# Kernel optimization log

Hardware: AMD Instinct MI355X
Metric: run time of the kernel (lower is better)

The kernel has to match this reference:

```python
import jax, jax.numpy as jnp
import numpy as np

B = 4096          # number of graphs
NPG = 148         # nodes per graph (fixed by ReadOut(num_nodes=148))
N = B * NPG       # total nodes = 606208
EPG = 592         # edges per graph (~avg degree 4: RNA backbone + base pairs)
E = B * EPG       # total edges = 2424832


def setup_inputs() -> dict:
    key = jax.random.key(0)
    ks = jax.random.split(key, 10)
    x = jax.random.normal(ks[0], (N, 4), jnp.float32)
    # edges confined within each graph via per-graph node offsets
    src = jax.random.randint(ks[1], (E,), 0, NPG, dtype=jnp.int32)
    dst = jax.random.randint(ks[2], (E,), 0, NPG, dtype=jnp.int32)
    offs = jnp.repeat(jnp.arange(B, dtype=jnp.int32) * NPG, EPG)
    edge_index = jnp.stack([src + offs, dst + offs], axis=0)
    batch = jnp.repeat(jnp.arange(B, dtype=jnp.int32), NPG)
    # GCNConv weights (glorot-ish) and biases: 4->16->32->64
    def glorot(k, fi, fo):
        return jax.random.normal(k, (fi, fo), jnp.float32) * np.sqrt(2.0 / (fi + fo)).astype(np.float32)
    W1 = glorot(ks[3], 4, 16); b1 = jnp.zeros((16,), jnp.float32)
    W2 = glorot(ks[4], 16, 32); b2 = jnp.zeros((32,), jnp.float32)
    W3 = glorot(ks[5], 32, 64); b3 = jnp.zeros((64,), jnp.float32)
    return {"x": x, "edge_index": edge_index, "batch": batch,
            "W1": W1, "b1": b1, "W2": W2, "b2": b2, "W3": W3, "b3": b3}


def gcn_conv(x, src, dst, W, b, n):
    """PyG GCNConv: x' = D^{-1/2}(A+I)D^{-1/2} (x W) + b."""
    h = x @ W                                   # [n, out]
    loop = jnp.arange(n, dtype=src.dtype)       # self loops
    s = jnp.concatenate([src, loop])
    d = jnp.concatenate([dst, loop])
    deg = jax.ops.segment_sum(jnp.ones_like(s, h.dtype), d, num_segments=n)
    dis = jnp.where(deg > 0, jax.lax.rsqrt(jnp.maximum(deg, 1e-12)), 0.0)
    norm = dis[s] * dis[d]                      # [n_edges_with_loops]
    msg = h[s] * norm[:, None]                  # gather + normalize
    return jax.ops.segment_sum(msg, d, num_segments=n) + b


def reference(x, edge_index, batch, W1, b1, W2, b2, W3, b3):
    src, dst = edge_index[0], edge_index[1]
    n = x.shape[0]
    # Dropout(p=0.1) is identity at inference time
    h = jax.nn.relu(gcn_conv(x, src, dst, W1, b1, n))
    h = jax.nn.relu(gcn_conv(h, src, dst, W2, b2, n))
    h = jax.nn.relu(gcn_conv(h, src, dst, W3, b3, n))
    # to_dense_batch with max_num_nodes=148: every graph has exactly 148 nodes
    # and `batch` is sorted block-constant, so dense batching == reshape.
    dense = h.reshape(B, NPG, h.shape[-1])      # [B, 148, 64]
    return dense.reshape(B, -1)                 # Flatten -> [B, 9472]
```

## Files before the change

### kernel.cpp

```cpp
#include <hip/hip_runtime.h>

#define NPG 148
#define EPG 592
#define NTHR 256
#define SA   40
#define MT   10

typedef _Float16 h8 __attribute__((ext_vector_type(8)));
typedef _Float16 h4 __attribute__((ext_vector_type(4)));
typedef float    f4 __attribute__((ext_vector_type(4)));

__device__ __forceinline__ float f16bits_to_f32(unsigned short u) {
    return (float)__builtin_bit_cast(_Float16, u);
}


template<int Fi, int Fo, int KC, int NTN, int MAXJ, int WROW, int BOFF, bool LAST>
__device__ __forceinline__ void layer(int t,
    _Float16* __restrict__ A16, const _Float16* __restrict__ Wt,
    const _Float16* __restrict__ s_bh, const unsigned int* __restrict__ s_csr,
    const unsigned short* __restrict__ s_row, const unsigned short* __restrict__ s_dis,
    float* __restrict__ gout)
{
    float a[KC][8];
    if (t < NPG) {
        const float dd = f16bits_to_f32(s_dis[t]);
        const char* selfb = reinterpret_cast<const char*>(A16) + t * (SA * 2);
        #pragma unroll
        for (int kc = 0; kc < KC; ++kc) {
            const h8 hv = *reinterpret_cast<const h8*>(selfb + kc * 16);
            #pragma unroll
            for (int u = 0; u < 8; ++u) a[kc][u] = dd * (float)hv[u];
        }
        int e  = s_row[t];
        const int e1 = s_row[t + 1];
        unsigned int pk = (e < e1) ? s_csr[e] : 0u;
        while (e < e1) {
            const unsigned int pknext = (e + 1 < e1) ? s_csr[e + 1] : 0u;
            const char* mb = reinterpret_cast<const char*>(A16) + (pk & 0xffffu);
            const float ds = f16bits_to_f32((unsigned short)(pk >> 16));
            #pragma unroll
            for (int kc = 0; kc < KC; ++kc) {
                const h8 m = *reinterpret_cast<const h8*>(mb + kc * 16);
                #pragma unroll
                for (int u = 0; u < 8; ++u) a[kc][u] = fmaf((float)m[u], ds, a[kc][u]);
            }
            pk = pknext;
            ++e;
        }
        #pragma unroll
        for (int kc = 0; kc < KC; ++kc)
            #pragma unroll
            for (int u = 0; u < 8; ++u) a[kc][u] *= dd;
    }
    __syncthreads();
    if (t < NPG) {
        char* selfb = reinterpret_cast<char*>(A16) + t * (SA * 2);
        #pragma unroll
        for (int kc = 0; kc < KC; ++kc) {
            h8 pv;
            #pragma unroll
            for (int u = 0; u < 8; ++u) pv[u] = (_Float16)a[kc][u];
            *reinterpret_cast<h8*>(selfb + kc * 16) = pv;
        }
    }
    __syncthreads();

    const int w   = t >> 6;
    const int l16 = t & 15;
    const int q   = (t >> 4) & 3;
    h8 af[MAXJ], bf[MAXJ];
    #pragma unroll
    for (int j = 0; j < MAXJ; ++j) {
        const int idx = w + 4 * j;
        if (idx < MT * NTN) {
            const int mt = idx / NTN, nt = idx % NTN;
            af[j] = *reinterpret_cast<const h8*>(&A16[(mt * 16 + l16) * SA + q * 8]);
            bf[j] = *reinterpret_cast<const h8*>(&Wt[(WROW + nt * 16 + l16) * SA + q * 8]);
        }
    }
    __syncthreads();
    #pragma unroll
    for (int j = 0; j < MAXJ; ++j) {
        const int idx = w + 4 * j;
        if (idx < MT * NTN) {
            const int mt = idx / NTN, nt = idx % NTN;
            f4 acc = {0.f, 0.f, 0.f, 0.f};
            acc = __builtin_amdgcn_mfma_f32_16x16x32_f16(af[j], bf[j], acc, 0, 0, 0);
            const int col  = nt * 16 + l16;
            const float bias = (float)s_bh[BOFF + col];
            #pragma unroll
            for (int rr = 0; rr < 4; ++rr) {
                const float v = fmaxf(acc[rr] + bias, 0.f);
                const int row = mt * 16 + q * 4 + rr;
                if (LAST) {
                    if (row < NPG) gout[row * 64 + col] = v;
                } else {
                    A16[row * SA + col] = (_Float16)v;
                }
            }
        }
    }
    if (!LAST) __syncthreads();
}

__global__ __launch_bounds__(256, 6)
void gcn_fused(const float* __restrict__ x,
               const int* __restrict__ esrc, const int* __restrict__ edst,
               const float* __restrict__ W1, const float* __restrict__ b1,
               const float* __restrict__ W2, const float* __restrict__ b2,
               const float* __restrict__ W3, const float* __restrict__ b3,
               float* __restrict__ out)
{
    __shared__ __align__(16) _Float16 A16[160 * SA];
    __shared__ __align__(16) _Float16 Wt[112 * SA];
    __shared__ _Float16 s_bh[112];
    __shared__ unsigned int s_csr[EPG];
    __shared__ unsigned short s_row[152];
    __shared__ unsigned short s_dis[NPG];
    __shared__ int s_cnt[NPG], s_cnt2[NPG];

    int* s_edge = reinterpret_cast<int*>(Wt);

    const int t  = threadIdx.x;
    const int g  = blockIdx.x;
    const int be = g * EPG;
    const int bn = g * NPG;

    if (t < NPG) { s_cnt[t] = 0; s_cnt2[t] = 0; }
    for (int e = t; e < EPG; e += NTHR) {
        const int s = esrc[be + e] - bn;
        const int d = edst[be + e] - bn;
        s_edge[e] = s | (d << 8);
    }
    __syncthreads();

    for (int e = t; e < EPG; e += NTHR)
        atomicAdd(&s_cnt[((unsigned)s_edge[e]) >> 8], 1);
    __syncthreads();

    if (t < NPG) {
        const float disf = rsqrtf((float)(s_cnt[t] + 1));
        s_dis[t] = __builtin_bit_cast(unsigned short, (_Float16)disf);
    }
    if (t < 64) {
        const int lane = t;
        int v0 = s_cnt[lane];
        int v1 = s_cnt[64 + lane];
        int v2 = (128 + lane < NPG) ? s_cnt[128 + lane] : 0;
        #pragma unroll
        for (int off = 1; off < 64; off <<= 1) {
            const int u0 = __shfl_up(v0, off);
            const int u1 = __shfl_up(v1, off);
            const int u2 = __shfl_up(v2, off);
            if (lane >= off) { v0 += u0; v1 += u1; v2 += u2; }
        }
        const int t0 = __shfl(v0, 63);
        const int t1 = __shfl(v1, 63);
        v1 += t0;
        v2 += t0 + t1;
        if (lane == 0) s_row[0] = 0;
        s_row[1 + lane]  = (unsigned short)v0;
        s_row[65 + lane] = (unsigned short)v1;
        if (128 + lane < NPG) s_row[129 + lane] = (unsigned short)v2;
    }
    __syncthreads();

    for (int e = t; e < EPG; e += NTHR) {
        const int pk = s_edge[e];
        const int s  = pk & 0xFF;
        const int d  = (unsigned)pk >> 8;
        const int pos = (int)s_row[d] + atomicAdd(&s_cnt2[d], 1);
        s_csr[pos] = (unsigned int)(s * (SA * 2)) | ((unsigned int)s_dis[s] << 16);
    }
    __syncthreads();

    for (int i = t; i < 160 * SA / 8; i += NTHR) reinterpret_cast<f4*>(A16)[i] = f4{0.f, 0.f, 0.f, 0.f};
    for (int i = t; i < 112 * SA / 8; i += NTHR) reinterpret_cast<f4*>(Wt)[i]  = f4{0.f, 0.f, 0.f, 0.f};
    __syncthreads();
    for (int i = t; i < 64;   i += NTHR) Wt[(i & 15) * SA + (i >> 4)]        = (_Float16)W1[i];
    for (int i = t; i < 512;  i += NTHR) Wt[(16 + (i & 31)) * SA + (i >> 5)] = (_Float16)W2[i];
    for (int i = t; i < 2048; i += NTHR) Wt[(48 + (i & 63)) * SA + (i >> 6)] = (_Float16)W3[i];
    if (t < 16)       s_bh[t] = (_Float16)b1[t];
    else if (t < 48)  s_bh[t] = (_Float16)b2[t - 16];
    else if (t < 112) s_bh[t] = (_Float16)b3[t - 48];
    if (t < NPG) {
        const float4 xv = reinterpret_cast<const float4*>(x)[bn + t];
        h4 p; p[0] = (_Float16)xv.x; p[1] = (_Float16)xv.y; p[2] = (_Float16)xv.z; p[3] = (_Float16)xv.w;
        *reinterpret_cast<h4*>(&A16[t * SA]) = p;
    }
    __syncthreads();

    float* gout = out + (size_t)bn * 64;
    layer< 4, 16,  1,  1,   3,    0,   0, false>(t, A16, Wt, s_bh, s_csr, s_row, s_dis, gout);
    layer<16, 32,  2,  2,   5,   16,  16, false>(t, A16, Wt, s_bh, s_csr, s_row, s_dis, gout);
    layer<32, 64,  4,  4,  10,   48,  48, true >(t, A16, Wt, s_bh, s_csr, s_row, s_dis, gout);
}

extern "C" void kernel_launch(void* const* d_in, const int* in_sizes, int n_in,
                              void* d_out, int out_size, void* d_ws, size_t ws_size,
                              hipStream_t stream)
{
    const float* x  = (const float*)d_in[0];
    const int*   ei = (const int*)d_in[1];
    const float* W1 = (const float*)d_in[3];
    const float* b1 = (const float*)d_in[4];
    const float* W2 = (const float*)d_in[5];
    const float* b2 = (const float*)d_in[6];
    const float* W3 = (const float*)d_in[7];
    const float* b3 = (const float*)d_in[8];
    float* out = (float*)d_out;

    const int N = in_sizes[0] / 4;
    const int B = N / NPG;
    const int E = in_sizes[1] / 2;

    gcn_fused<<<B, NTHR, 0, stream>>>(x, ei, ei + E, W1, b1, W2, b2, W3, b3, out);
}
```

Before: 64.96 us.

## Aggregate neighbors directly into MFMA fragments and overlap weight staging with CSR build

Each thread now gathers and normalizes one node's 8-feature chunk straight into the MFMA A-fragment registers. This removes the intermediate write-back of aggregated features to shared memory and two barriers per layer. Weight loading is restructured so each B fragment is loaded once per column tile and reused across the M tiles, and the activation row stride shrinks from 40 to 36 halves. Zeroing and loading W1/W2, biases and x are moved ahead of the CSR build, and W3 loading happens without a separate barrier. The risks are relying on the layer-1 barriers to order the W3 writes, possible bank conflicts at the new stride, and uneven gather work across lanes.

```diff
diff --git a/kernel.cpp b/kernel.cpp
--- a/kernel.cpp
+++ b/kernel.cpp
@@ -3,100 +3,84 @@
 #define NPG 148
 #define EPG 592
 #define NTHR 256
-#define SA   40
+#define SA   36
+#define SW   40
 #define MT   10
 
 typedef _Float16 h8 __attribute__((ext_vector_type(8)));
 typedef _Float16 h4 __attribute__((ext_vector_type(4)));
 typedef float    f4 __attribute__((ext_vector_type(4)));
 
-__device__ __forceinline__ float f16bits_to_f32(unsigned short u) {
+__device__ __forceinline__ float f16b(unsigned short u) {
     return (float)__builtin_bit_cast(_Float16, u);
 }
 
 
-template<int Fi, int Fo, int KC, int NTN, int MAXJ, int WROW, int BOFF, bool LAST>
+template<int Fi, int Fo, int NTN, int WROW, int BOFF, bool LAST>
 __device__ __forceinline__ void layer(int t,
     _Float16* __restrict__ A16, const _Float16* __restrict__ Wt,
     const _Float16* __restrict__ s_bh, const unsigned int* __restrict__ s_csr,
     const unsigned short* __restrict__ s_row, const unsigned short* __restrict__ s_dis,
     float* __restrict__ gout)
 {
-    float a[KC][8];
-    if (t < NPG) {
-        const float dd = f16bits_to_f32(s_dis[t]);
-        const char* selfb = reinterpret_cast<const char*>(A16) + t * (SA * 2);
-        #pragma unroll
-        for (int kc = 0; kc < KC; ++kc) {
-            const h8 hv = *reinterpret_cast<const h8*>(selfb + kc * 16);
-            #pragma unroll
-            for (int u = 0; u < 8; ++u) a[kc][u] = dd * (float)hv[u];
-        }
-        int e  = s_row[t];
-        const int e1 = s_row[t + 1];
-        unsigned int pk = (e < e1) ? s_csr[e] : 0u;
-        while (e < e1) {
-            const unsigned int pknext = (e + 1 < e1) ? s_csr[e + 1] : 0u;
-            const char* mb = reinterpret_cast<const char*>(A16) + (pk & 0xffffu);
-            const float ds = f16bits_to_f32((unsigned short)(pk >> 16));
-            #pragma unroll
-            for (int kc = 0; kc < KC; ++kc) {
-                const h8 m = *reinterpret_cast<const h8*>(mb + kc * 16);
-                #pragma unroll
-                for (int u = 0; u < 8; ++u) a[kc][u] = fmaf((float)m[u], ds, a[kc][u]);
-            }
-            pk = pknext;
-            ++e;
-        }
-        #pragma unroll
-        for (int kc = 0; kc < KC; ++kc)
-            #pragma unroll
-            for (int u = 0; u < 8; ++u) a[kc][u] *= dd;
-    }
-    __syncthreads();
-    if (t < NPG) {
-        char* selfb = reinterpret_cast<char*>(A16) + t * (SA * 2);
-        #pragma unroll
-        for (int kc = 0; kc < KC; ++kc) {
-            h8 pv;
-            #pragma unroll
-            for (int u = 0; u < 8; ++u) pv[u] = (_Float16)a[kc][u];
-            *reinterpret_cast<h8*>(selfb + kc * 16) = pv;
-        }
-    }
-    __syncthreads();
-
     const int w   = t >> 6;
     const int l16 = t & 15;
     const int q   = (t >> 4) & 3;
-    h8 af[MAXJ], bf[MAXJ];
+    constexpr int KQA = (Fi + 7) / 8;
+
+    h8 af[3];
+    const char* baseq = reinterpret_cast<const char*>(A16) + q * 16;
     #pragma unroll
-    for (int j = 0; j < MAXJ; ++j) {
-        const int idx = w + 4 * j;
-        if (idx < MT * NTN) {
-            const int mt = idx / NTN, nt = idx % NTN;
-            af[j] = *reinterpret_cast<const h8*>(&A16[(mt * 16 + l16) * SA + q * 8]);
-            bf[j] = *reinterpret_cast<const h8*>(&Wt[(WROW + nt * 16 + l16) * SA + q * 8]);
+    for (int j = 0; j < 3; ++j) {
+        h8 z = {(_Float16)0, (_Float16)0, (_Float16)0, (_Float16)0,
+                (_Float16)0, (_Float16)0, (_Float16)0, (_Float16)0};
+        af[j] = z;
+        const int mt   = w + 4 * j;
+        const int node = mt * 16 + l16;
+        if (mt < MT && q < KQA && node < NPG) {
+            const float dd = f16b(s_dis[node]);
+            const h8 hv = *reinterpret_cast<const h8*>(baseq + node * (SA * 2));
+            float a[8];
+            #pragma unroll
+            for (int u = 0; u < 8; ++u) a[u] = dd * (float)hv[u];
+            int e = s_row[node];
+            const int e1 = s_row[node + 1];
+            unsigned int pk = (e < e1) ? s_csr[e] : 0u;
+            while (e < e1) {
+                const unsigned int pn = (e + 1 < e1) ? s_csr[e + 1] : 0u;
+                const h8 m = *reinterpret_cast<const h8*>(baseq + (pk & 0xffffu));
+                const float ds = f16b((unsigned short)(pk >> 16));
+                #pragma unroll
+                for (int u = 0; u < 8; ++u) a[u] = fmaf((float)m[u], ds, a[u]);
+                pk = pn;
+                ++e;
+            }
+            #pragma unroll
+            for (int u = 0; u < 8; ++u) af[j][u] = (_Float16)(a[u] * dd);
         }
     }
     __syncthreads();
+
     #pragma unroll
-    for (int j = 0; j < MAXJ; ++j) {
-        const int idx = w + 4 * j;
-        if (idx < MT * NTN) {
-            const int mt = idx / NTN, nt = idx % NTN;
-            f4 acc = {0.f, 0.f, 0.f, 0.f};
-            acc = __builtin_amdgcn_mfma_f32_16x16x32_f16(af[j], bf[j], acc, 0, 0, 0);
-            const int col  = nt * 16 + l16;
-            const float bias = (float)s_bh[BOFF + col];
-            #pragma unroll
-            for (int rr = 0; rr < 4; ++rr) {
-                const float v = fmaxf(acc[rr] + bias, 0.f);
-                const int row = mt * 16 + q * 4 + rr;
-                if (LAST) {
-                    if (row < NPG) gout[row * 64 + col] = v;
-                } else {
-                    A16[row * SA + col] = (_Float16)v;
+    for (int nt = 0; nt < NTN; ++nt) {
+        const h8 bf = *reinterpret_cast<const h8*>(&Wt[(WROW + nt * 16 + l16) * SW + q * 8]);
+        const int col = nt * 16 + l16;
+        const float bias = (float)s_bh[BOFF + col];
+        #pragma unroll
+        for (int j = 0; j < 3; ++j) {
+            const int mt = w + 4 * j;
+            if (mt < MT) {
+                f4 acc = {0.f, 0.f, 0.f, 0.f};
+                acc = __builtin_amdgcn_mfma_f32_16x16x32_f16(af[j], bf, acc, 0, 0, 0);
+                #pragma unroll
+                for (int rr = 0; rr < 4; ++rr) {
+                    const float v = fmaxf(acc[rr] + bias, 0.f);
+                    const int row = mt * 16 + q * 4 + rr;
+                    if (LAST) {
+                        if (row < NPG) gout[row * 64 + col] = v;
+                    } else {
+                        A16[row * SA + col] = (_Float16)v;
+                    }
                 }
             }
         }
@@ -113,20 +97,35 @@
                float* __restrict__ out)
 {
     __shared__ __align__(16) _Float16 A16[160 * SA];
-    __shared__ __align__(16) _Float16 Wt[112 * SA];
+    __shared__ __align__(16) _Float16 Wt[112 * SW];
     __shared__ _Float16 s_bh[112];
     __shared__ unsigned int s_csr[EPG];
     __shared__ unsigned short s_row[152];
-    __shared__ unsigned short s_dis[NPG];
+    __shared__ unsigned short s_dis[148];
     __shared__ int s_cnt[NPG], s_cnt2[NPG];
 
-    int* s_edge = reinterpret_cast<int*>(Wt);
+    int* s_edge = reinterpret_cast<int*>(Wt + 48 * SW);
 
     const int t  = threadIdx.x;
     const int g  = blockIdx.x;
     const int be = g * EPG;
     const int bn = g * NPG;
 
+    for (int i = t; i < 160 * SA / 8; i += NTHR)
+        reinterpret_cast<f4*>(A16)[i] = f4{0.f, 0.f, 0.f, 0.f};
+    for (int i = t; i < 224; i += NTHR) {
+        const int r = i / 14, c = 2 + i % 14;
+        reinterpret_cast<unsigned int*>(Wt)[r * (SW / 2) + c] = 0u;
+    }
+    for (int i = t; i < 256; i += NTHR) {
+        const int r = 16 + i / 8, c = 8 + i % 8;
+        reinterpret_cast<unsigned int*>(Wt)[r * (SW / 2) + c] = 0u;
+    }
+    for (int i = t; i < 64;  i += NTHR) Wt[(i & 15) * SW + (i >> 4)]        = (_Float16)W1[i];
+    for (int i = t; i < 512; i += NTHR) Wt[(16 + (i & 31)) * SW + (i >> 5)] = (_Float16)W2[i];
+    if (t < 16)       s_bh[t] = (_Float16)b1[t];
+    else if (t < 48)  s_bh[t] = (_Float16)b2[t - 16];
+    else if (t < 112) s_bh[t] = (_Float16)b3[t - 48];
     if (t < NPG) { s_cnt[t] = 0; s_cnt2[t] = 0; }
     for (int e = t; e < EPG; e += NTHR) {
         const int s = esrc[be + e] - bn;
@@ -142,6 +141,9 @@
     if (t < NPG) {
         const float disf = rsqrtf((float)(s_cnt[t] + 1));
         s_dis[t] = __builtin_bit_cast(unsigned short, (_Float16)disf);
+        const float4 xv = reinterpret_cast<const float4*>(x)[bn + t];
+        h4 p; p[0] = (_Float16)xv.x; p[1] = (_Float16)xv.y; p[2] = (_Float16)xv.z; p[3] = (_Float16)xv.w;
+        *reinterpret_cast<h4*>(&A16[t * SA]) = p;
     }
     if (t < 64) {
         const int lane = t;
@@ -175,26 +177,13 @@
     }
     __syncthreads();
 
-    for (int i = t; i < 160 * SA / 8; i += NTHR) reinterpret_cast<f4*>(A16)[i] = f4{0.f, 0.f, 0.f, 0.f};
-    for (int i = t; i < 112 * SA / 8; i += NTHR) reinterpret_cast<f4*>(Wt)[i]  = f4{0.f, 0.f, 0.f, 0.f};
-    __syncthreads();
-    for (int i = t; i < 64;   i += NTHR) Wt[(i & 15) * SA + (i >> 4)]        = (_Float16)W1[i];
-    for (int i = t; i < 512;  i += NTHR) Wt[(16 + (i & 31)) * SA + (i >> 5)] = (_Float16)W2[i];
-    for (int i = t; i < 2048; i += NTHR) Wt[(48 + (i & 63)) * SA + (i >> 6)] = (_Float16)W3[i];
-    if (t < 16)       s_bh[t] = (_Float16)b1[t];
-    else if (t < 48)  s_bh[t] = (_Float16)b2[t - 16];
-    else if (t < 112) s_bh[t] = (_Float16)b3[t - 48];
-    if (t < NPG) {
-        const float4 xv = reinterpret_cast<const float4*>(x)[bn + t];
-        h4 p; p[0] = (_Float16)xv.x; p[1] = (_Float16)xv.y; p[2] = (_Float16)xv.z; p[3] = (_Float16)xv.w;
-        *reinterpret_cast<h4*>(&A16[t * SA]) = p;
-    }
-    __syncthreads();
+    for (int i = t; i < 2048; i += NTHR)
+        Wt[(48 + (i & 63)) * SW + (i >> 6)] = (_Float16)W3[i];
 
     float* gout = out + (size_t)bn * 64;
-    layer< 4, 16,  1,  1,   3,    0,   0, false>(t, A16, Wt, s_bh, s_csr, s_row, s_dis, gout);
-    layer<16, 32,  2,  2,   5,   16,  16, false>(t, A16, Wt, s_bh, s_csr, s_row, s_dis, gout);
-    layer<32, 64,  4,  4,  10,   48,  48, true >(t, A16, Wt, s_bh, s_csr, s_row, s_dis, gout);
+    layer< 4, 16,  1,    0,   0, false>(t, A16, Wt, s_bh, s_csr, s_row, s_dis, gout);
+    layer<16, 32,  2,   16,  16, false>(t, A16, Wt, s_bh, s_csr, s_row, s_dis, gout);
+    layer<32, 64,  4,   48,  48, true >(t, A16, Wt, s_bh, s_csr, s_row, s_dis, gout);
 }
 
 extern "C" void kernel_launch(void* const* d_in, const int* in_sizes, int n_in,
```

Result: slower. 83.03 us (+27.8%).

## Degree-sort aggregation threads, use packed fp16 math, and merge setup phases

Applied to the files above, without the earlier changes.

Aggregation now runs in packed fp16 vector arithmetic instead of per-element fp32 FMAs. Nodes are reassigned to threads in degree-sorted order through a counting sort (s_meta), which aims to cut wavefront divergence in the edge loop. The setup phases are reorganised: edges are kept in registers, weight and x loading overlaps with degree counting, and several barriers are dropped. The A16 row stride shrinks to 36 halves, which changes the LDS bank pattern. fp16 accumulation loses precision compared with the previous fp32 accumulation.

```diff
diff --git a/kernel.cpp b/kernel.cpp
--- a/kernel.cpp
+++ b/kernel.cpp
@@ -3,66 +3,59 @@
 #define NPG 148
 #define EPG 592
 #define NTHR 256
-#define SA   40
+#define SA   36
+#define SW   40
 #define MT   10
 
 typedef _Float16 h8 __attribute__((ext_vector_type(8)));
 typedef _Float16 h4 __attribute__((ext_vector_type(4)));
 typedef float    f4 __attribute__((ext_vector_type(4)));
-
-__device__ __forceinline__ float f16bits_to_f32(unsigned short u) {
-    return (float)__builtin_bit_cast(_Float16, u);
+typedef unsigned int u32;
+
+__device__ __forceinline__ h8 bcast_pk(u32 p) {
+    uint4 q = {p, p, p, p};
+    return __builtin_bit_cast(h8, q);
 }
 
 
 template<int Fi, int Fo, int KC, int NTN, int MAXJ, int WROW, int BOFF, bool LAST>
 __device__ __forceinline__ void layer(int t,
     _Float16* __restrict__ A16, const _Float16* __restrict__ Wt,
-    const _Float16* __restrict__ s_bh, const unsigned int* __restrict__ s_csr,
-    const unsigned short* __restrict__ s_row, const unsigned short* __restrict__ s_dis,
-    float* __restrict__ gout)
+    const _Float16* __restrict__ s_bh, const u32* __restrict__ s_csr,
+    const uint2* __restrict__ s_meta, float* __restrict__ gout)
 {
-    float a[KC][8];
-    if (t < NPG) {
-        const float dd = f16bits_to_f32(s_dis[t]);
-        const char* selfb = reinterpret_cast<const char*>(A16) + t * (SA * 2);
-        #pragma unroll
-        for (int kc = 0; kc < KC; ++kc) {
-            const h8 hv = *reinterpret_cast<const h8*>(selfb + kc * 16);
+    h8 a[KC];
+    int off_self = 0;
+    if (t < NPG) {
+        const uint2 me = s_meta[t];
+        off_self = (int)(me.x & 0xffffu);
+        const h8 ddv = bcast_pk((me.x & 0xffff0000u) | (me.x >> 16));
+        const char* base = reinterpret_cast<const char*>(A16) + off_self;
+        #pragma unroll
+        for (int kc = 0; kc < KC; ++kc)
+            a[kc] = *reinterpret_cast<const h8*>(base + kc * 16) * ddv;
+        int e = (int)(me.y & 0xffffu);
+        const int e1 = (int)(me.y >> 16);
+        u32 pk = (e < e1) ? s_csr[e] : 0u;
+        while (e < e1) {
+            const u32 pn = (e + 1 < e1) ? s_csr[e + 1] : 0u;
+            const char* mb = reinterpret_cast<const char*>(A16) + (pk & 0xffffu);
+            const h8 dsv = bcast_pk((pk & 0xffff0000u) | (pk >> 16));
             #pragma unroll
-            for (int u = 0; u < 8; ++u) a[kc][u] = dd * (float)hv[u];
-        }
-        int e  = s_row[t];
-        const int e1 = s_row[t + 1];
-        unsigned int pk = (e < e1) ? s_csr[e] : 0u;
-        while (e < e1) {
-            const unsigned int pknext = (e + 1 < e1) ? s_csr[e + 1] : 0u;
-            const char* mb = reinterpret_cast<const char*>(A16) + (pk & 0xffffu);
-            const float ds = f16bits_to_f32((unsigned short)(pk >> 16));
-            #pragma unroll
-            for (int kc = 0; kc < KC; ++kc) {
-                const h8 m = *reinterpret_cast<const h8*>(mb + kc * 16);
-                #pragma unroll
-                for (int u = 0; u < 8; ++u) a[kc][u] = fmaf((float)m[u], ds, a[kc][u]);
-            }
-            pk = pknext;
+            for (int kc = 0; kc < KC; ++kc)
+                a[kc] += *reinterpret_cast<const h8*>(mb + kc * 16) * dsv;
+            pk = pn;
             ++e;
         }
         #pragma unroll
+        for (int kc = 0; kc < KC; ++kc) a[kc] *= ddv;
+    }
+    __syncthreads();
+    if (t < NPG) {
+        char* base = reinterpret_cast<char*>(A16) + off_self;
+        #pragma unroll
         for (int kc = 0; kc < KC; ++kc)
-            #pragma unroll
-            for (int u = 0; u < 8; ++u) a[kc][u] *= dd;
-    }
-    __syncthreads();
-    if (t < NPG) {
-        char* selfb = reinterpret_cast<char*>(A16) + t * (SA * 2);
-        #pragma unroll
-        for (int kc = 0; kc < KC; ++kc) {
-            h8 pv;
-            #pragma unroll
-            for (int u = 0; u < 8; ++u) pv[u] = (_Float16)a[kc][u];
-            *reinterpret_cast<h8*>(selfb + kc * 16) = pv;
-        }
+            *reinterpret_cast<h8*>(base + kc * 16) = a[kc];
     }
     __syncthreads();
 
@@ -76,7 +69,7 @@
         if (idx < MT * NTN) {
             const int mt = idx / NTN, nt = idx % NTN;
             af[j] = *reinterpret_cast<const h8*>(&A16[(mt * 16 + l16) * SA + q * 8]);
-            bf[j] = *reinterpret_cast<const h8*>(&Wt[(WROW + nt * 16 + l16) * SA + q * 8]);
+            bf[j] = *reinterpret_cast<const h8*>(&Wt[(WROW + nt * 16 + l16) * SW + q * 8]);
         }
     }
     __syncthreads();
@@ -113,36 +106,60 @@
                float* __restrict__ out)
 {
     __shared__ __align__(16) _Float16 A16[160 * SA];
-    __shared__ __align__(16) _Float16 Wt[112 * SA];
+    __shared__ __align__(16) _Float16 Wt[112 * SW];
     __shared__ _Float16 s_bh[112];
-    __shared__ unsigned int s_csr[EPG];
+    __shared__ u32 s_csr[EPG];
     __shared__ unsigned short s_row[152];
     __shared__ unsigned short s_dis[NPG];
+    __shared__ uint2 s_meta[NPG];
     __shared__ int s_cnt[NPG], s_cnt2[NPG];
-
-    int* s_edge = reinterpret_cast<int*>(Wt);
+    __shared__ int s_hist[64], s_boff[64], s_bcnt[64];
 
     const int t  = threadIdx.x;
     const int g  = blockIdx.x;
     const int be = g * EPG;
     const int bn = g * NPG;
 
+    for (int i = t; i < 160 * SA / 8; i += NTHR)
+        reinterpret_cast<f4*>(A16)[i] = f4{0.f, 0.f, 0.f, 0.f};
+    for (int i = t; i < 112 * SW / 8; i += NTHR)
+        reinterpret_cast<f4*>(Wt)[i] = f4{0.f, 0.f, 0.f, 0.f};
     if (t < NPG) { s_cnt[t] = 0; s_cnt2[t] = 0; }
-    for (int e = t; e < EPG; e += NTHR) {
-        const int s = esrc[be + e] - bn;
-        const int d = edst[be + e] - bn;
-        s_edge[e] = s | (d << 8);
-    }
-    __syncthreads();
-
-    for (int e = t; e < EPG; e += NTHR)
-        atomicAdd(&s_cnt[((unsigned)s_edge[e]) >> 8], 1);
-    __syncthreads();
-
-    if (t < NPG) {
-        const float disf = rsqrtf((float)(s_cnt[t] + 1));
-        s_dis[t] = __builtin_bit_cast(unsigned short, (_Float16)disf);
-    }
+    if (t < 64)  { s_hist[t] = 0; s_bcnt[t] = 0; }
+    __syncthreads();
+
+    u32 epk[3];
+    #pragma unroll
+    for (int k = 0; k < 3; ++k) {
+        const int e = t + k * NTHR;
+        epk[k] = 0xffffffffu;
+        if (e < EPG) {
+            const int s = esrc[be + e] - bn;
+            const int d = edst[be + e] - bn;
+            epk[k] = (u32)(s | (d << 8));
+            atomicAdd(&s_cnt[d], 1);
+        }
+    }
+    for (int i = t; i < 64;   i += NTHR) Wt[(i & 15) * SW + (i >> 4)]        = (_Float16)W1[i];
+    for (int i = t; i < 512;  i += NTHR) Wt[(16 + (i & 31)) * SW + (i >> 5)] = (_Float16)W2[i];
+    for (int i = t; i < 2048; i += NTHR) Wt[(48 + (i & 63)) * SW + (i >> 6)] = (_Float16)W3[i];
+    if (t < 16)       s_bh[t] = (_Float16)b1[t];
+    else if (t < 48)  s_bh[t] = (_Float16)b2[t - 16];
+    else if (t < 112) s_bh[t] = (_Float16)b3[t - 48];
+    if (t < NPG) {
+        const float4 xv = reinterpret_cast<const float4*>(x)[bn + t];
+        h4 p; p[0] = (_Float16)xv.x; p[1] = (_Float16)xv.y; p[2] = (_Float16)xv.z; p[3] = (_Float16)xv.w;
+        *reinterpret_cast<h4*>(&A16[t * SA]) = p;
+    }
+    __syncthreads();
+
+    if (t < NPG) {
+        const int deg = s_cnt[t];
+        s_dis[t] = __builtin_bit_cast(unsigned short, (_Float16)rsqrtf((float)(deg + 1)));
+        atomicAdd(&s_hist[min(deg, 63)], 1);
+    }
+    __syncthreads();
+
     if (t < 64) {
         const int lane = t;
         int v0 = s_cnt[lane];
@@ -163,38 +180,41 @@
         s_row[1 + lane]  = (unsigned short)v0;
         s_row[65 + lane] = (unsigned short)v1;
         if (128 + lane < NPG) s_row[129 + lane] = (unsigned short)v2;
-    }
-    __syncthreads();
-
-    for (int e = t; e < EPG; e += NTHR) {
-        const int pk = s_edge[e];
-        const int s  = pk & 0xFF;
-        const int d  = (unsigned)pk >> 8;
-        const int pos = (int)s_row[d] + atomicAdd(&s_cnt2[d], 1);
-        s_csr[pos] = (unsigned int)(s * (SA * 2)) | ((unsigned int)s_dis[s] << 16);
-    }
-    __syncthreads();
-
-    for (int i = t; i < 160 * SA / 8; i += NTHR) reinterpret_cast<f4*>(A16)[i] = f4{0.f, 0.f, 0.f, 0.f};
-    for (int i = t; i < 112 * SA / 8; i += NTHR) reinterpret_cast<f4*>(Wt)[i]  = f4{0.f, 0.f, 0.f, 0.f};
-    __syncthreads();
-    for (int i = t; i < 64;   i += NTHR) Wt[(i & 15) * SA + (i >> 4)]        = (_Float16)W1[i];
-    for (int i = t; i < 512;  i += NTHR) Wt[(16 + (i & 31)) * SA + (i >> 5)] = (_Float16)W2[i];
-    for (int i = t; i < 2048; i += NTHR) Wt[(48 + (i & 63)) * SA + (i >> 6)] = (_Float16)W3[i];
-    if (t < 16)       s_bh[t] = (_Float16)b1[t];
-    else if (t < 48)  s_bh[t] = (_Float16)b2[t - 16];
-    else if (t < 112) s_bh[t] = (_Float16)b3[t - 48];
-    if (t < NPG) {
-        const float4 xv = reinterpret_cast<const float4*>(x)[bn + t];
-        h4 p; p[0] = (_Float16)xv.x; p[1] = (_Float16)xv.y; p[2] = (_Float16)xv.z; p[3] = (_Float16)xv.w;
-        *reinterpret_cast<h4*>(&A16[t * SA]) = p;
+    } else if (t < 128) {
+        const int lane = t - 64;
+        const int orig = s_hist[lane];
+        int v = orig;
+        #pragma unroll
+        for (int off = 1; off < 64; off <<= 1) {
+            const int u = __shfl_up(v, off);
+            if (lane >= off) v += u;
+        }
+        s_boff[lane] = v - orig;
+    }
+    __syncthreads();
+
+    #pragma unroll
+    for (int k = 0; k < 3; ++k) {
+        if (epk[k] != 0xffffffffu) {
+            const int s = epk[k] & 0xff;
+            const int d = (epk[k] >> 8) & 0xff;
+            const int pos = (int)s_row[d] + atomicAdd(&s_cnt2[d], 1);
+            s_csr[pos] = (u32)(s * (SA * 2)) | ((u32)s_dis[s] << 16);
+        }
+    }
+    if (t < NPG) {
+        const int deg = s_cnt[t];
+        const int b   = min(deg, 63);
+        const int p   = s_boff[b] + atomicAdd(&s_bcnt[b], 1);
+        s_meta[p] = make_uint2((u32)(t * (SA * 2)) | ((u32)s_dis[t] << 16),
+                               (u32)s_row[t] | ((u32)s_row[t + 1] << 16));
     }
     __syncthreads();
 
     float* gout = out + (size_t)bn * 64;
-    layer< 4, 16,  1,  1,   3,    0,   0, false>(t, A16, Wt, s_bh, s_csr, s_row, s_dis, gout);
-    layer<16, 32,  2,  2,   5,   16,  16, false>(t, A16, Wt, s_bh, s_csr, s_row, s_dis, gout);
-    layer<32, 64,  4,  4,  10,   48,  48, true >(t, A16, Wt, s_bh, s_csr, s_row, s_dis, gout);
+    layer< 4, 16,  1,  1,   3,    0,   0, false>(t, A16, Wt, s_bh, s_csr, s_meta, gout);
+    layer<16, 32,  2,  2,   5,   16,  16, false>(t, A16, Wt, s_bh, s_csr, s_meta, gout);
+    layer<32, 64,  4,  4,  10,   48,  48, true >(t, A16, Wt, s_bh, s_csr, s_meta, gout);
 }
 
 extern "C" void kernel_launch(void* const* d_in, const int* in_sizes, int n_in,
```

New measurement: 108.9 us. 1.68x slower.

## Process two graphs per block and merge setup phases to cut barriers

Applied to the files above, without the earlier changes.

Each 512-thread block now handles two graphs, one per 256-thread half, so the weight transpose and bias loads are shared across two graphs. Edge packing and degree counting are fused into one pass that keeps the packed edges in registers, and the separate zeroing and weight-load phases are merged, which removes several block-wide barriers. The activation row stride drops to 36 halves, presumably to change the LDS bank pattern and cut footprint. The risks are that 16-byte vector LDS accesses on 72-byte rows are no longer 16-byte aligned, that barriers now stall both graphs together, and that the larger LDS footprint per block could lower occupancy.

```diff
diff --git a/kernel.cpp b/kernel.cpp
--- a/kernel.cpp
+++ b/kernel.cpp
@@ -2,50 +2,53 @@
 
 #define NPG 148
 #define EPG 592
-#define NTHR 256
-#define SA   40
+#define NTHR 512
+#define GPB  2
+#define SA   36
+#define SW   40
 #define MT   10
 
 typedef _Float16 h8 __attribute__((ext_vector_type(8)));
 typedef _Float16 h4 __attribute__((ext_vector_type(4)));
 typedef float    f4 __attribute__((ext_vector_type(4)));
-
-__device__ __forceinline__ float f16bits_to_f32(unsigned short u) {
+typedef unsigned int u32;
+
+__device__ __forceinline__ float f16b(unsigned short u) {
     return (float)__builtin_bit_cast(_Float16, u);
 }
 
 
 template<int Fi, int Fo, int KC, int NTN, int MAXJ, int WROW, int BOFF, bool LAST>
-__device__ __forceinline__ void layer(int t,
+__device__ __forceinline__ void layer(int tl,
     _Float16* __restrict__ A16, const _Float16* __restrict__ Wt,
-    const _Float16* __restrict__ s_bh, const unsigned int* __restrict__ s_csr,
+    const _Float16* __restrict__ s_bh, const u32* __restrict__ s_csr,
     const unsigned short* __restrict__ s_row, const unsigned short* __restrict__ s_dis,
     float* __restrict__ gout)
 {
     float a[KC][8];
-    if (t < NPG) {
-        const float dd = f16bits_to_f32(s_dis[t]);
-        const char* selfb = reinterpret_cast<const char*>(A16) + t * (SA * 2);
+    if (tl < NPG) {
+        const float dd = f16b(s_dis[tl]);
+        const char* selfb = reinterpret_cast<const char*>(A16) + tl * (SA * 2);
         #pragma unroll
         for (int kc = 0; kc < KC; ++kc) {
             const h8 hv = *reinterpret_cast<const h8*>(selfb + kc * 16);
             #pragma unroll
             for (int u = 0; u < 8; ++u) a[kc][u] = dd * (float)hv[u];
         }
-        int e  = s_row[t];
-        const int e1 = s_row[t + 1];
-        unsigned int pk = (e < e1) ? s_csr[e] : 0u;
+        int e  = s_row[tl];
+        const int e1 = s_row[tl + 1];
+        u32 pk = (e < e1) ? s_csr[e] : 0u;
         while (e < e1) {
-            const unsigned int pknext = (e + 1 < e1) ? s_csr[e + 1] : 0u;
+            const u32 pn = (e + 1 < e1) ? s_csr[e + 1] : 0u;
             const char* mb = reinterpret_cast<const char*>(A16) + (pk & 0xffffu);
-            const float ds = f16bits_to_f32((unsigned short)(pk >> 16));
+            const float ds = f16b((unsigned short)(pk >> 16));
             #pragma unroll
             for (int kc = 0; kc < KC; ++kc) {
                 const h8 m = *reinterpret_cast<const h8*>(mb + kc * 16);
                 #pragma unroll
                 for (int u = 0; u < 8; ++u) a[kc][u] = fmaf((float)m[u], ds, a[kc][u]);
             }
-            pk = pknext;
+            pk = pn;
             ++e;
         }
         #pragma unroll
@@ -54,8 +57,8 @@
             for (int u = 0; u < 8; ++u) a[kc][u] *= dd;
     }
     __syncthreads();
-    if (t < NPG) {
-        char* selfb = reinterpret_cast<char*>(A16) + t * (SA * 2);
+    if (tl < NPG) {
+        char* selfb = reinterpret_cast<char*>(A16) + tl * (SA * 2);
         #pragma unroll
         for (int kc = 0; kc < KC; ++kc) {
             h8 pv;
@@ -66,9 +69,9 @@
     }
     __syncthreads();
 
-    const int w   = t >> 6;
-    const int l16 = t & 15;
-    const int q   = (t >> 4) & 3;
+    const int w   = tl >> 6;
+    const int l16 = tl & 15;
+    const int q   = (tl >> 4) & 3;
     h8 af[MAXJ], bf[MAXJ];
     #pragma unroll
     for (int j = 0; j < MAXJ; ++j) {
@@ -76,7 +79,7 @@
         if (idx < MT * NTN) {
             const int mt = idx / NTN, nt = idx % NTN;
             af[j] = *reinterpret_cast<const h8*>(&A16[(mt * 16 + l16) * SA + q * 8]);
-            bf[j] = *reinterpret_cast<const h8*>(&Wt[(WROW + nt * 16 + l16) * SA + q * 8]);
+            bf[j] = *reinterpret_cast<const h8*>(&Wt[(WROW + nt * 16 + l16) * SW + q * 8]);
         }
     }
     __syncthreads();
@@ -104,7 +107,7 @@
     if (!LAST) __syncthreads();
 }
 
-__global__ __launch_bounds__(256, 6)
+__global__ __launch_bounds__(NTHR, 8)
 void gcn_fused(const float* __restrict__ x,
                const int* __restrict__ esrc, const int* __restrict__ edst,
                const float* __restrict__ W1, const float* __restrict__ b1,
@@ -112,42 +115,61 @@
                const float* __restrict__ W3, const float* __restrict__ b3,
                float* __restrict__ out)
 {
-    __shared__ __align__(16) _Float16 A16[160 * SA];
-    __shared__ __align__(16) _Float16 Wt[112 * SA];
+    __shared__ __align__(16) _Float16 A16[GPB][160 * SA];
+    __shared__ __align__(16) _Float16 Wt[112 * SW];
     __shared__ _Float16 s_bh[112];
-    __shared__ unsigned int s_csr[EPG];
-    __shared__ unsigned short s_row[152];
-    __shared__ unsigned short s_dis[NPG];
-    __shared__ int s_cnt[NPG], s_cnt2[NPG];
-
-    int* s_edge = reinterpret_cast<int*>(Wt);
+    __shared__ u32 s_csr[GPB][EPG];
+    __shared__ unsigned short s_row[GPB][152];
+    __shared__ unsigned short s_dis[GPB][NPG];
+    __shared__ int s_cnt[GPB][NPG], s_cnt2[GPB][NPG];
 
     const int t  = threadIdx.x;
-    const int g  = blockIdx.x;
+    const int gl = t >> 8;
+    const int tl = t & 255;
+    const int g  = blockIdx.x * GPB + gl;
     const int be = g * EPG;
     const int bn = g * NPG;
 
-    if (t < NPG) { s_cnt[t] = 0; s_cnt2[t] = 0; }
-    for (int e = t; e < EPG; e += NTHR) {
-        const int s = esrc[be + e] - bn;
-        const int d = edst[be + e] - bn;
-        s_edge[e] = s | (d << 8);
-    }
-    __syncthreads();
-
-    for (int e = t; e < EPG; e += NTHR)
-        atomicAdd(&s_cnt[((unsigned)s_edge[e]) >> 8], 1);
-    __syncthreads();
-
-    if (t < NPG) {
-        const float disf = rsqrtf((float)(s_cnt[t] + 1));
-        s_dis[t] = __builtin_bit_cast(unsigned short, (_Float16)disf);
-    }
-    if (t < 64) {
-        const int lane = t;
-        int v0 = s_cnt[lane];
-        int v1 = s_cnt[64 + lane];
-        int v2 = (128 + lane < NPG) ? s_cnt[128 + lane] : 0;
+    for (int i = t; i < GPB * 160 * SA / 8; i += NTHR)
+        reinterpret_cast<f4*>(&A16[0][0])[i] = f4{0.f, 0.f, 0.f, 0.f};
+    for (int i = t; i < 112 * SW / 8; i += NTHR)
+        reinterpret_cast<f4*>(Wt)[i] = f4{0.f, 0.f, 0.f, 0.f};
+    if (tl < NPG) { s_cnt[gl][tl] = 0; s_cnt2[gl][tl] = 0; }
+    __syncthreads();
+
+    u32 epk[3];
+    #pragma unroll
+    for (int k = 0; k < 3; ++k) {
+        const int e = tl + k * 256;
+        epk[k] = 0xffffffffu;
+        if (e < EPG) {
+            const int s = esrc[be + e] - bn;
+            const int d = edst[be + e] - bn;
+            epk[k] = (u32)(s | (d << 8));
+            atomicAdd(&s_cnt[gl][d], 1);
+        }
+    }
+    for (int i = t; i < 64;   i += NTHR) Wt[(i & 15) * SW + (i >> 4)]        = (_Float16)W1[i];
+    for (int i = t; i < 512;  i += NTHR) Wt[(16 + (i & 31)) * SW + (i >> 5)] = (_Float16)W2[i];
+    for (int i = t; i < 2048; i += NTHR) Wt[(48 + (i & 63)) * SW + (i >> 6)] = (_Float16)W3[i];
+    if (t < 16)       s_bh[t] = (_Float16)b1[t];
+    else if (t < 48)  s_bh[t] = (_Float16)b2[t - 16];
+    else if (t < 112) s_bh[t] = (_Float16)b3[t - 48];
+    if (tl < NPG) {
+        const float4 xv = reinterpret_cast<const float4*>(x)[bn + tl];
+        h4 p; p[0] = (_Float16)xv.x; p[1] = (_Float16)xv.y; p[2] = (_Float16)xv.z; p[3] = (_Float16)xv.w;
+        *reinterpret_cast<h4*>(&A16[gl][tl * SA]) = p;
+    }
+    __syncthreads();
+
+    if (tl < NPG)
+        s_dis[gl][tl] = __builtin_bit_cast(unsigned short,
+                                           (_Float16)rsqrtf((float)(s_cnt[gl][tl] + 1)));
+    if (tl < 64) {
+        const int lane = tl;
+        int v0 = s_cnt[gl][lane];
+        int v1 = s_cnt[gl][64 + lane];
+        int v2 = (128 + lane < NPG) ? s_cnt[gl][128 + lane] : 0;
         #pragma unroll
         for (int off = 1; off < 64; off <<= 1) {
             const int u0 = __shfl_up(v0, off);
@@ -159,42 +181,28 @@
         const int t1 = __shfl(v1, 63);
         v1 += t0;
         v2 += t0 + t1;
-        if (lane == 0) s_row[0] = 0;
-        s_row[1 + lane]  = (unsigned short)v0;
-        s_row[65 + lane] = (unsigned short)v1;
-        if (128 + lane < NPG) s_row[129 + lane] = (unsigned short)v2;
-    }
-    __syncthreads();
-
-    for (int e = t; e < EPG; e += NTHR) {
-        const int pk = s_edge[e];
-        const int s  = pk & 0xFF;
-        const int d  = (unsigned)pk >> 8;
-        const int pos = (int)s_row[d] + atomicAdd(&s_cnt2[d], 1);
-        s_csr[pos] = (unsigned int)(s * (SA * 2)) | ((unsigned int)s_dis[s] << 16);
-    }
-    __syncthreads();
-
-    for (int i = t; i < 160 * SA / 8; i += NTHR) reinterpret_cast<f4*>(A16)[i] = f4{0.f, 0.f, 0.f, 0.f};
-    for (int i = t; i < 112 * SA / 8; i += NTHR) reinterpret_cast<f4*>(Wt)[i]  = f4{0.f, 0.f, 0.f, 0.f};
-    __syncthreads();
-    for (int i = t; i < 64;   i += NTHR) Wt[(i & 15) * SA + (i >> 4)]        = (_Float16)W1[i];
-    for (int i = t; i < 512;  i += NTHR) Wt[(16 + (i & 31)) * SA + (i >> 5)] = (_Float16)W2[i];
-    for (int i = t; i < 2048; i += NTHR) Wt[(48 + (i & 63)) * SA + (i >> 6)] = (_Float16)W3[i];
-    if (t < 16)       s_bh[t] = (_Float16)b1[t];
-    else if (t < 48)  s_bh[t] = (_Float16)b2[t - 16];
-    else if (t < 112) s_bh[t] = (_Float16)b3[t - 48];
-    if (t < NPG) {
-        const float4 xv = reinterpret_cast<const float4*>(x)[bn + t];
-        h4 p; p[0] = (_Float16)xv.x; p[1] = (_Float16)xv.y; p[2] = (_Float16)xv.z; p[3] = (_Float16)xv.w;
-        *reinterpret_cast<h4*>(&A16[t * SA]) = p;
+        if (lane == 0) s_row[gl][0] = 0;
+        s_row[gl][1 + lane]  = (unsigned short)v0;
+        s_row[gl][65 + lane] = (unsigned short)v1;
+        if (128 + lane < NPG) s_row[gl][129 + lane] = (unsigned short)v2;
+    }
+    __syncthreads();
+
+    #pragma unroll
+    for (int k = 0; k < 3; ++k) {
+        if (epk[k] != 0xffffffffu) {
+            const int s = epk[k] & 0xff;
+            const int d = (epk[k] >> 8) & 0xff;
+            const int pos = (int)s_row[gl][d] + atomicAdd(&s_cnt2[gl][d], 1);
+            s_csr[gl][pos] = (u32)(s * (SA * 2)) | ((u32)s_dis[gl][s] << 16);
+        }
     }
     __syncthreads();
 
     float* gout = out + (size_t)bn * 64;
-    layer< 4, 16,  1,  1,   3,    0,   0, false>(t, A16, Wt, s_bh, s_csr, s_row, s_dis, gout);
-    layer<16, 32,  2,  2,   5,   16,  16, false>(t, A16, Wt, s_bh, s_csr, s_row, s_dis, gout);
-    layer<32, 64,  4,  4,  10,   48,  48, true >(t, A16, Wt, s_bh, s_csr, s_row, s_dis, gout);
+    layer< 4, 16,  1,  1,   3,    0,   0, false>(tl, A16[gl], Wt, s_bh, s_csr[gl], s_row[gl], s_dis[gl], gout);
+    layer<16, 32,  2,  2,   5,   16,  16, false>(tl, A16[gl], Wt, s_bh, s_csr[gl], s_row[gl], s_dis[gl], gout);
+    layer<32, 64,  4,  4,  10,   48,  48, true >(tl, A16[gl], Wt, s_bh, s_csr[gl], s_row[gl], s_dis[gl], gout);
 }
 
 extern "C" void kernel_launch(void* const* d_in, const int* in_sizes, int n_in,
@@ -215,5 +223,5 @@
     const int B = N / NPG;
     const int E = in_sizes[1] / 2;
 
-    gcn_fused<<<B, NTHR, 0, stream>>>(x, ei, ei + E, W1, b1, W2, b2, W3, b3, out);
-}
+    gcn_fused<<<B / GPB, NTHR, 0, stream>>>(x, ei, ei + E, W1, b1, W2, b2, W3, b3, out);
+}
```

After: 108.3 us. 1.67x slower.
